# Optimization experiments

Hardware: AMD Instinct MI355X
Metric: run time of the kernel (lower is better)

## Reference

```python
import jax, jax.numpy as jnp
import numpy as np

B, L, C = 2, 2048, 2048
H, HKV, D = 16, 4, 128  # heads, kv heads, head_dim
G = H // HKV            # GQA group size
NEG = -1e9


def rms_norm(x, w, eps=1e-6):
    # FastRMSNorm: compute in fp32, scale by weight, cast back
    xf = x.astype(jnp.float32)
    y = xf * jax.lax.rsqrt(jnp.mean(xf * xf, axis=-1, keepdims=True) + eps) * w
    return y.astype(x.dtype)


def apply_rope(t, cos, sin):
    # t: (B, h, L, D); cos/sin: (L, D//2) broadcast to (1,1,L,D//2)
    t1, t2 = jnp.split(t, 2, axis=-1)
    c = cos[None, None]
    s = sin[None, None]
    return jnp.concatenate([t1 * c - t2 * s, t2 * c + t1 * s], axis=-1)


def setup_inputs() -> dict:
    key = jax.random.key(0)
    ks = jax.random.split(key, 8)
    x = jax.random.normal(ks[0], (B, L, C), jnp.float32)
    Wq = jax.random.normal(ks[1], (H * D, C), jnp.float32) * 0.02
    Wk = jax.random.normal(ks[2], (HKV * D, C), jnp.float32) * 0.02
    Wv = jax.random.normal(ks[3], (HKV * D, C), jnp.float32) * 0.02
    Wo = jax.random.normal(ks[4], (C, H * D), jnp.float32) * 0.02
    q_norm_w = jnp.ones((D,), jnp.float32)
    k_norm_w = jnp.ones((D,), jnp.float32)
    pos = jnp.arange(L, dtype=jnp.float32)[:, None]
    inv_freq = 1.0 / (10000.0 ** (jnp.arange(0, D, 2, dtype=jnp.float32) / D))
    ang = pos * inv_freq[None, :]            # (L, D//2)
    rope_cos = jnp.cos(ang)
    rope_sin = jnp.sin(ang)
    # VAR-style block-causal visibility: 8 blocks of 256, query block i sees key blocks <= i
    blk = jnp.arange(L) // 256
    vis = blk[None, :] <= blk[:, None]       # (L, L) bool
    attn_bias = jnp.where(vis, 0.0, NEG).astype(jnp.float32)[None, None]  # (1,1,L,L)
    return dict(x=x, Wq=Wq, Wk=Wk, Wv=Wv, Wo=Wo, q_norm_w=q_norm_w,
                k_norm_w=k_norm_w, rope_cos=rope_cos, rope_sin=rope_sin,
                attn_bias=attn_bias)


def reference(x, Wq, Wk, Wv, Wo, q_norm_w, k_norm_w, rope_cos, rope_sin, attn_bias):
    b, l, c = x.shape
    # fused projections -> (B, h, L, D)
    q = rms_norm((x @ Wq.T).reshape(b, l, H, D), q_norm_w).transpose(0, 2, 1, 3)
    k = rms_norm((x @ Wk.T).reshape(b, l, HKV, D), k_norm_w).transpose(0, 2, 1, 3)
    v = (x @ Wv.T).reshape(b, l, HKV, D).transpose(0, 2, 1, 3)
    q = apply_rope(q, rope_cos, rope_sin)
    k = apply_rope(k, rope_cos, rope_sin)
    scale = D ** -0.5
    # GQA: group query heads over kv heads
    qg = q.reshape(b, HKV, G, l, D)
    scores = jnp.einsum('bkgqd,bkKd->bkgqK', qg, k) * scale
    scores = scores + attn_bias[:, :, None]  # broadcast (1,1,1,L,L)
    probs = jax.nn.softmax(scores, axis=-1)
    out = jnp.einsum('bkgqK,bkKd->bkgqd', probs, v)
    out = out.reshape(b, H, l, D).transpose(0, 2, 1, 3).reshape(b, l, H * D)
    return out @ Wo.T
```

## Files before the change

### kernel.cpp

```cpp
#include <hip/hip_runtime.h>

#define B_ 2
#define L_ 2048
#define C_ 2048
#define H_ 16
#define HKV_ 4
#define D_ 128
#define G_ (H_ / HKV_)
#define TOK_ (B_ * L_)
#define NQKV_ 3072

typedef __bf16 bf16;
typedef __bf16 bf16x4 __attribute__((ext_vector_type(4)));
typedef __bf16 bf16x8 __attribute__((ext_vector_type(8)));
typedef float f32x4 __attribute__((ext_vector_type(4)));

__device__ inline void gload16(const void* g, void* l) {
  __builtin_amdgcn_global_load_lds(
      (const __attribute__((address_space(1))) void*)g,
      (__attribute__((address_space(3))) void*)l, 16, 0, 0);
}

__global__ void cvt_bf16(const float* __restrict__ in, bf16* __restrict__ out, int n4) {
  int stride = gridDim.x * blockDim.x;
  for (int j = blockIdx.x * blockDim.x + threadIdx.x; j < n4; j += stride) {
    float4 v = reinterpret_cast<const float4*>(in)[j];
    bf16x4 o = {(bf16)v.x, (bf16)v.y, (bf16)v.z, (bf16)v.w};
    reinterpret_cast<bf16x4*>(out)[j] = o;
  }
}

template <bool OUT_F32>
__global__ __launch_bounds__(256) void gemm_bt(
    const bf16* __restrict__ A, const bf16* __restrict__ Bm,
    void* __restrict__ Cm, int M, int N, int K) {
  __shared__ __align__(16) bf16 sA[128 * 32];
  __shared__ __align__(16) bf16 sB[128 * 32];
  const int tid = threadIdx.x;
  const int row0 = blockIdx.x * 128, col0 = blockIdx.y * 128;
  const int wid = tid >> 6, lane = tid & 63;
  const int wr = wid >> 1, wc = wid & 1;
  const int l15 = lane & 15, kk = (lane >> 4) * 8;
  f32x4 acc[4][4] = {};
  const int nk = K / 32;
  const int f0 = tid;
  const int r0 = f0 >> 2, c0 = f0 & 3;
  const int f1 = 256 + tid;
  const int r1 = f1 >> 2, c1 = f1 & 3;
  const int ldsA0 = (wid * 64) * 8, ldsA1 = (256 + wid * 64) * 8;
  for (int kt = 0; kt < nk; ++kt) {
    __syncthreads();
    gload16(A + (size_t)(row0 + r0) * K + kt * 32 + c0 * 8, sA + ldsA0);
    gload16(A + (size_t)(row0 + r1) * K + kt * 32 + c1 * 8, sA + ldsA1);
    gload16(Bm + (size_t)(col0 + r0) * K + kt * 32 + c0 * 8, sB + ldsA0);
    gload16(Bm + (size_t)(col0 + r1) * K + kt * 32 + c1 * 8, sB + ldsA1);
    __syncthreads();
    bf16x8 af[4], bfr[4];
#pragma unroll
    for (int m = 0; m < 4; ++m)
      af[m] = *reinterpret_cast<const bf16x8*>(sA + (wr * 64 + m * 16 + l15) * 32 + kk);
#pragma unroll
    for (int n = 0; n < 4; ++n)
      bfr[n] = *reinterpret_cast<const bf16x8*>(sB + (wc * 64 + n * 16 + l15) * 32 + kk);
#pragma unroll
    for (int m = 0; m < 4; ++m)
#pragma unroll
      for (int n = 0; n < 4; ++n)
        acc[m][n] = __builtin_amdgcn_mfma_f32_16x16x32_bf16(af[m], bfr[n], acc[m][n], 0, 0, 0);
  }
#pragma unroll
  for (int m = 0; m < 4; ++m)
#pragma unroll
    for (int n = 0; n < 4; ++n)
#pragma unroll
      for (int r = 0; r < 4; ++r) {
        int row = row0 + wr * 64 + m * 16 + (lane >> 4) * 4 + r;
        int col = col0 + wc * 64 + n * 16 + l15;
        if constexpr (OUT_F32)
          reinterpret_cast<float*>(Cm)[(size_t)row * N + col] = acc[m][n][r];
        else
          reinterpret_cast<bf16*>(Cm)[(size_t)row * N + col] = (bf16)acc[m][n][r];
      }
}

__global__ void k_norm_rope(const bf16* __restrict__ proj,
                            const float* __restrict__ normw,
                            const float* __restrict__ cosb,
                            const float* __restrict__ sinb,
                            bf16* __restrict__ out) {
  int wid = (blockIdx.x * blockDim.x + threadIdx.x) >> 6;
  int lane = threadIdx.x & 63;
  int head = wid & 3, tok = wid >> 2;
  int b = tok / L_, l = tok % L_;
  const bf16* p = proj + (size_t)tok * NQKV_ + H_ * D_ + head * D_;
  float t1 = (float)p[lane];
  float t2 = (float)p[lane + 64];
  float ss = t1 * t1 + t2 * t2;
#pragma unroll
  for (int off = 32; off; off >>= 1) ss += __shfl_xor(ss, off);
  float r = rsqrtf(ss * (1.0f / 128.0f) + 1e-6f);
  float n1 = t1 * r * normw[lane];
  float n2 = t2 * r * normw[lane + 64];
  float c = cosb[l * 64 + lane], s = sinb[l * 64 + lane];
  bf16* q = out + (((size_t)b * HKV_ + head) * L_ + l) * D_;
  q[lane] = (bf16)(n1 * c - n2 * s);
  q[lane + 64] = (bf16)(n2 * c + n1 * s);
}

__global__ __launch_bounds__(256) void v_transpose(const bf16* __restrict__ proj,
                                                   bf16* __restrict__ vt) {
  __shared__ __align__(16) bf16 sT[64 * 136];
  const int t = threadIdx.x;
  const int l0 = blockIdx.x * 64;
  const int bk = blockIdx.y;
  const bf16* src = proj + (size_t)((bk >> 2) * L_ + l0) * NQKV_ + (H_ + HKV_) * D_ + (bk & 3) * D_;
#pragma unroll
  for (int c = 0; c < 4; ++c) {
    int idx = c * 256 + t;
    int l = idx >> 4, dc = idx & 15;
    bf16x8 v = *reinterpret_cast<const bf16x8*>(src + (size_t)l * NQKV_ + dc * 8);
    *reinterpret_cast<bf16x8*>((char*)sT + l * 272 + ((dc ^ (l >> 3)) << 4)) = v;
  }
  __syncthreads();
  bf16* dst = vt + (size_t)bk * D_ * L_ + l0;
#pragma unroll
  for (int c = 0; c < 4; ++c) {
    int idx = c * 256 + t;
    int d = idx >> 3, lg = idx & 7;
    bf16x8 o;
#pragma unroll
    for (int j = 0; j < 8; ++j) {
      int l = lg * 8 + j;
      o[j] = *reinterpret_cast<const bf16*>((char*)sT + l * 272 + (((d >> 3) ^ lg) << 4) + (d & 7) * 2);
    }
    *reinterpret_cast<bf16x8*>(dst + (size_t)d * L_ + lg * 8) = o;
  }
}

__global__ __launch_bounds__(512, 4) void attn_fused(
    const bf16* __restrict__ QKV,
    const bf16* __restrict__ Kn,
    const bf16* __restrict__ Vt,
    const float* __restrict__ qnw,
    const float* __restrict__ cosb, const float* __restrict__ sinb,
    bf16* __restrict__ AO) {
  __shared__ __align__(16) bf16 sK[2][64 * 128];
  __shared__ __align__(16) bf16 sV[2][64 * 128];
  __shared__ __align__(16) bf16 sP[8 * 16 * 64];
  const int tid = threadIdx.x;
  const int wid = tid >> 6, lane = tid & 63;
  const int bid = blockIdx.x;
  const int bk = bid & 7;
  const int qt = (bid < 256) ? (bid >> 3) : 63 - ((bid - 256) >> 3);
  const int b = bk >> 2;
  const int hl = wid & 3, qs = wid >> 2;
  const int h = (bk & 3) * G_ + hl;
  const int qrow0 = qt * 32 + qs * 16;
  const int l15 = lane & 15, g4 = lane >> 4, kk = g4 * 8;
  const int swz = (l15 & 7) << 4;

  const int qrow = qrow0 + l15;
  const bf16* qsrc = QKV + (size_t)(b * L_ + qrow) * NQKV_ + h * D_;
  float t[4][8];
  float ss = 0.f;
#pragma unroll
  for (int c = 0; c < 4; ++c) {
    bf16x8 v = *reinterpret_cast<const bf16x8*>(qsrc + c * 32 + kk);
#pragma unroll
    for (int j = 0; j < 8; ++j) { t[c][j] = (float)v[j]; ss += t[c][j] * t[c][j]; }
  }

  const int kr0 = tid >> 4, kc0 = tid & 15;
  const int kr1 = 32 + kr0;
  const int vr0 = tid >> 3, vc0 = tid & 7;
  const int vr1 = 64 + vr0;
  const bf16* kb = Kn + (size_t)bk * L_ * D_;
  const bf16* vb = Vt + (size_t)bk * D_ * (size_t)L_;
  const bf16* kp0 = kb + (size_t)kr0 * D_ + ((kc0 ^ (kr0 & 7)) * 8);
  const bf16* kp1 = kb + (size_t)kr1 * D_ + ((kc0 ^ (kr1 & 7)) * 8);
  const bf16* vp0 = vb + (size_t)vr0 * L_ + ((vc0 ^ (vr0 & 7)) * 8);
  const bf16* vp1 = vb + (size_t)vr1 * L_ + ((vc0 ^ (vr1 & 7)) * 8);

  const int ntiles = ((qt >> 3) + 1) * 4;
  gload16(kp0, &sK[0][tid * 8]);
  gload16(kp1, &sK[0][(512 + tid) * 8]);
  gload16(vp0, &sV[0][tid * 8]);
  gload16(vp1, &sV[0][(512 + tid) * 8]);

  constexpr float SCL = 0.12752650038632816f;
  ss += __shfl_xor(ss, 16);
  ss += __shfl_xor(ss, 32);
  const float rr = rsqrtf(ss * (1.0f / 128.0f) + 1e-6f);
  bf16x8 qf[4];
#pragma unroll
  for (int c = 0; c < 2; ++c)
#pragma unroll
    for (int j = 0; j < 8; ++j) {
      int i = c * 32 + kk + j;
      float n1 = t[c][j] * rr * qnw[i];
      float n2 = t[c + 2][j] * rr * qnw[i + 64];
      float cs = cosb[qrow * 64 + i], sn = sinb[qrow * 64 + i];
      qf[c][j] = (bf16)((n1 * cs - n2 * sn) * SCL);
      qf[c + 2][j] = (bf16)((n2 * cs + n1 * sn) * SCL);
    }

  char* myP = (char*)(sP + wid * 16 * 64);
  f32x4 acc[8] = {};
  float mref = -1e30f, lpart = 0.f;

  __syncthreads();

  auto tile_step = [&](const bf16* sKc, const bf16* sVc, bf16* sKn_, bf16* sVn_,
                       int ktNext, bool doPref) {
    if (doPref) {
      gload16(kp0 + (size_t)ktNext * 64 * D_, &sKn_[tid * 8]);
      gload16(kp1 + (size_t)ktNext * 64 * D_, &sKn_[(512 + tid) * 8]);
      gload16(vp0 + ktNext * 64, &sVn_[tid * 8]);
      gload16(vp1 + ktNext * 64, &sVn_[(512 + tid) * 8]);
    }
    const char* cK = (const char*)sKc;
    const char* cV = (const char*)sVc;
    f32x4 s[4];
    __builtin_amdgcn_s_setprio(1);
#pragma unroll
    for (int n = 0; n < 4; ++n) {
      f32x4 st = {};
#pragma unroll
      for (int c = 0; c < 4; ++c) {
        int byte = (n * 16 + l15) * 256 + ((((c << 2) + g4) ^ (l15 & 7)) << 4);
        bf16x8 kf = *reinterpret_cast<const bf16x8*>(cK + byte);
        st = __builtin_amdgcn_mfma_f32_16x16x32_bf16(kf, qf[c], st, 0, 0, 0);
      }
      s[n] = st;
    }
    __builtin_amdgcn_s_setprio(0);
    float pm = fmaxf(fmaxf(s[0][0], s[0][1]), fmaxf(s[0][2], s[0][3]));
#pragma unroll
    for (int n = 1; n < 4; ++n)
      pm = fmaxf(pm, fmaxf(fmaxf(s[n][0], s[n][1]), fmaxf(s[n][2], s[n][3])));
    if (!__all(pm <= mref + 8.f)) {
      pm = fmaxf(pm, __shfl_xor(pm, 16));
      pm = fmaxf(pm, __shfl_xor(pm, 32));
      float mnew = fmaxf(mref, pm);
      float resc = exp2f(mref - mnew);
      mref = mnew;
      lpart *= resc;
#pragma unroll
      for (int f = 0; f < 8; ++f) acc[f] *= resc;
    }
#pragma unroll
    for (int n = 0; n < 4; ++n)
#pragma unroll
      for (int r = 0; r < 4; ++r) {
        float p = exp2f(s[n][r] - mref);
        s[n][r] = p;
        lpart += p;
      }
#pragma unroll
    for (int n = 0; n < 4; ++n) {
      bf16x4 pw = {(bf16)s[n][0], (bf16)s[n][1], (bf16)s[n][2], (bf16)s[n][3]};
      *reinterpret_cast<bf16x4*>(myP + l15 * 128 + (((n << 5) + (g4 << 3)) ^ swz)) = pw;
    }
    bf16x8 pf0 = *reinterpret_cast<const bf16x8*>(myP + l15 * 128 + ((g4 << 4) ^ swz));
    bf16x8 pf1 = *reinterpret_cast<const bf16x8*>(myP + l15 * 128 + ((64 + (g4 << 4)) ^ swz));
    __builtin_amdgcn_s_setprio(1);
#pragma unroll
    for (int f = 0; f < 8; ++f) {
      int d = f * 16 + l15;
      bf16x8 vf0 = *reinterpret_cast<const bf16x8*>(cV + d * 128 + ((g4 ^ (l15 & 7)) << 4));
      acc[f] = __builtin_amdgcn_mfma_f32_16x16x32_bf16(vf0, pf0, acc[f], 0, 0, 0);
      bf16x8 vf1 = *reinterpret_cast<const bf16x8*>(cV + d * 128 + (((4 + g4) ^ (l15 & 7)) << 4));
      acc[f] = __builtin_amdgcn_mfma_f32_16x16x32_bf16(vf1, pf1, acc[f], 0, 0, 0);
    }
    __builtin_amdgcn_s_setprio(0);
    __syncthreads();
  };

  for (int kt = 0; kt < ntiles; kt += 2) {
    tile_step(sK[0], sV[0], sK[1], sV[1], kt + 1, true);
    tile_step(sK[1], sV[1], sK[0], sV[0], kt + 2, kt + 2 < ntiles);
  }

  lpart += __shfl_xor(lpart, 16);
  lpart += __shfl_xor(lpart, 32);
  const float rinv = 1.f / lpart;
  bf16* aop = AO + ((size_t)(b * L_ + qrow0 + l15) * H_ + h) * D_ + (g4 << 2);
#pragma unroll
  for (int f = 0; f < 8; ++f) {
    bf16x4 o = {(bf16)(acc[f][0] * rinv), (bf16)(acc[f][1] * rinv),
                (bf16)(acc[f][2] * rinv), (bf16)(acc[f][3] * rinv)};
    *reinterpret_cast<bf16x4*>(aop + f * 16) = o;
  }
}

extern "C" void kernel_launch(void* const* d_in, const int* in_sizes, int n_in,
                              void* d_out, int out_size, void* d_ws, size_t ws_size,
                              hipStream_t stream) {
  const float* x = (const float*)d_in[0];
  const float* Wq = (const float*)d_in[1];
  const float* Wk = (const float*)d_in[2];
  const float* Wv = (const float*)d_in[3];
  const float* Wo = (const float*)d_in[4];
  const float* qnw = (const float*)d_in[5];
  const float* knw = (const float*)d_in[6];
  const float* rc = (const float*)d_in[7];
  const float* rs = (const float*)d_in[8];
  float* out = (float*)d_out;

  char* ws = (char*)d_ws;
  bf16* xb = (bf16*)ws;    ws += (size_t)TOK_ * C_ * 2;
  bf16* wqb = (bf16*)ws;   ws += (size_t)(H_ * D_) * C_ * 2;
  bf16* wkb = (bf16*)ws;   ws += (size_t)(HKV_ * D_) * C_ * 2;
  bf16* wvb = (bf16*)ws;   ws += (size_t)(HKV_ * D_) * C_ * 2;
  bf16* wob = (bf16*)ws;   ws += (size_t)C_ * (H_ * D_) * 2;
  bf16* qkv = (bf16*)ws;   ws += (size_t)TOK_ * NQKV_ * 2;
  bf16* Kb = (bf16*)ws;    ws += (size_t)TOK_ * HKV_ * D_ * 2;
  bf16* Vtb = (bf16*)ws;   ws += (size_t)TOK_ * HKV_ * D_ * 2;
  bf16* AOb = xb;

  auto cvt = [&](const float* src, bf16* dst, size_t n) {
    int n4 = (int)(n / 4);
    int grid = (n4 + 255) / 256;
    if (grid > 4096) grid = 4096;
    cvt_bf16<<<grid, 256, 0, stream>>>(src, dst, n4);
  };
  cvt(x, xb, (size_t)TOK_ * C_);
  cvt(Wq, wqb, (size_t)H_ * D_ * C_);
  cvt(Wk, wkb, (size_t)HKV_ * D_ * C_);
  cvt(Wv, wvb, (size_t)HKV_ * D_ * C_);
  cvt(Wo, wob, (size_t)C_ * H_ * D_);

  gemm_bt<false><<<dim3(TOK_ / 128, NQKV_ / 128), 256, 0, stream>>>(
      xb, wqb, qkv, TOK_, NQKV_, C_);

  k_norm_rope<<<(TOK_ * HKV_) / 4, 256, 0, stream>>>(qkv, knw, rc, rs, Kb);
  v_transpose<<<dim3(L_ / 64, B_ * HKV_), 256, 0, stream>>>(qkv, Vtb);

  attn_fused<<<512, 512, 0, stream>>>(qkv, Kb, Vtb, qnw, rc, rs, AOb);

  gemm_bt<true><<<dim3(TOK_ / 128, C_ / 128), 256, 0, stream>>>(
      AOb, wob, out, TOK_, C_, H_ * D_);
}
```

Before: 218.5 us.

## Rewrite GEMM with 256x128 tiles, triple-buffered async LDS loads, swizzled layout

The bf16 GEMM used for the QKV and output projections now uses 512-thread blocks with 256x128 tiles and a K step of 64. Global-to-LDS loads are triple-buffered and prefetched two steps ahead, with vmcnt waits replacing the two full syncthreads per iteration. The LDS layout uses an XOR swizzle to avoid bank conflicts, and MFMA sections get raised wave priority. This aims to hide memory latency and cut barrier overhead, at the cost of much more LDS (about 144KB) and fewer blocks in the grid.

Measured after the change: 232.9 us. 6.6% more time.

```diff
diff --git a/kernel.cpp b/kernel.cpp
--- a/kernel.cpp
+++ b/kernel.cpp
@@ -31,51 +31,80 @@
 }
 
 template <bool OUT_F32>
-__global__ __launch_bounds__(256) void gemm_bt(
+__global__ __launch_bounds__(512) void gemm_bt(
     const bf16* __restrict__ A, const bf16* __restrict__ Bm,
     void* __restrict__ Cm, int M, int N, int K) {
-  __shared__ __align__(16) bf16 sA[128 * 32];
-  __shared__ __align__(16) bf16 sB[128 * 32];
+  __shared__ __align__(16) bf16 sA[3][256 * 64];
+  __shared__ __align__(16) bf16 sB[3][128 * 64];
   const int tid = threadIdx.x;
-  const int row0 = blockIdx.x * 128, col0 = blockIdx.y * 128;
   const int wid = tid >> 6, lane = tid & 63;
-  const int wr = wid >> 1, wc = wid & 1;
-  const int l15 = lane & 15, kk = (lane >> 4) * 8;
+  const int row0 = blockIdx.x * 256, col0 = blockIdx.y * 128;
+  const int wwr = wid & 3, wwc = wid >> 2;
+  const int l15 = lane & 15, g4 = lane >> 4;
+  const int ra = tid >> 3, ca = tid & 7;
+  const bf16* gA = A + (size_t)(row0 + ra) * K + ((ca ^ (ra & 7)) << 3);
+  const bf16* gB = Bm + (size_t)(col0 + ra) * K + ((ca ^ (ra & 7)) << 3);
+  const int ldsOff = tid * 8;
+  const int nk = K >> 6;
+
+  auto stage = [&](int kt, int slot) {
+    const bf16* a = gA + kt * 64;
+    const bf16* b = gB + kt * 64;
+#pragma unroll
+    for (int j = 0; j < 4; ++j)
+      gload16(a + (size_t)(64 * j) * K, &sA[slot][ldsOff + j * 64 * 64]);
+#pragma unroll
+    for (int j = 0; j < 2; ++j)
+      gload16(b + (size_t)(64 * j) * K, &sB[slot][ldsOff + j * 64 * 64]);
+  };
+
   f32x4 acc[4][4] = {};
-  const int nk = K / 32;
-  const int f0 = tid;
-  const int r0 = f0 >> 2, c0 = f0 & 3;
-  const int f1 = 256 + tid;
-  const int r1 = f1 >> 2, c1 = f1 & 3;
-  const int ldsA0 = (wid * 64) * 8, ldsA1 = (256 + wid * 64) * 8;
+  stage(0, 0);
+  stage(1, 1);
+  asm volatile("s_waitcnt vmcnt(6)" ::: "memory");
+  __builtin_amdgcn_s_barrier();
+  __builtin_amdgcn_sched_barrier(0);
+
+  int slot = 0;
   for (int kt = 0; kt < nk; ++kt) {
-    __syncthreads();
-    gload16(A + (size_t)(row0 + r0) * K + kt * 32 + c0 * 8, sA + ldsA0);
-    gload16(A + (size_t)(row0 + r1) * K + kt * 32 + c1 * 8, sA + ldsA1);
-    gload16(Bm + (size_t)(col0 + r0) * K + kt * 32 + c0 * 8, sB + ldsA0);
-    gload16(Bm + (size_t)(col0 + r1) * K + kt * 32 + c1 * 8, sB + ldsA1);
-    __syncthreads();
-    bf16x8 af[4], bfr[4];
-#pragma unroll
-    for (int m = 0; m < 4; ++m)
-      af[m] = *reinterpret_cast<const bf16x8*>(sA + (wr * 64 + m * 16 + l15) * 32 + kk);
+    int s2 = slot + 2; if (s2 >= 3) s2 -= 3;
+    if (kt + 2 < nk) stage(kt + 2, s2);
+    const bf16* cA = sA[slot];
+    const bf16* cB = sB[slot];
+#pragma unroll
+    for (int kh = 0; kh < 2; ++kh) {
+      bf16x8 af[4], bfr[4];
+      const int ch = (((kh << 2) + g4) ^ (l15 & 7)) << 3;
+#pragma unroll
+      for (int m = 0; m < 4; ++m)
+        af[m] = *reinterpret_cast<const bf16x8*>(cA + (wwr * 64 + m * 16 + l15) * 64 + ch);
+#pragma unroll
+      for (int n = 0; n < 4; ++n)
+        bfr[n] = *reinterpret_cast<const bf16x8*>(cB + (wwc * 64 + n * 16 + l15) * 64 + ch);
+      __builtin_amdgcn_s_setprio(1);
+#pragma unroll
+      for (int m = 0; m < 4; ++m)
+#pragma unroll
+        for (int n = 0; n < 4; ++n)
+          acc[m][n] = __builtin_amdgcn_mfma_f32_16x16x32_bf16(af[m], bfr[n], acc[m][n], 0, 0, 0);
+      __builtin_amdgcn_s_setprio(0);
+    }
+    if (kt + 2 < nk)
+      asm volatile("s_waitcnt vmcnt(6)" ::: "memory");
+    else
+      asm volatile("s_waitcnt vmcnt(0)" ::: "memory");
+    __builtin_amdgcn_s_barrier();
+    __builtin_amdgcn_sched_barrier(0);
+    slot = (slot + 1 == 3) ? 0 : slot + 1;
+  }
+#pragma unroll
+  for (int m = 0; m < 4; ++m)
 #pragma unroll
     for (int n = 0; n < 4; ++n)
-      bfr[n] = *reinterpret_cast<const bf16x8*>(sB + (wc * 64 + n * 16 + l15) * 32 + kk);
-#pragma unroll
-    for (int m = 0; m < 4; ++m)
-#pragma unroll
-      for (int n = 0; n < 4; ++n)
-        acc[m][n] = __builtin_amdgcn_mfma_f32_16x16x32_bf16(af[m], bfr[n], acc[m][n], 0, 0, 0);
-  }
-#pragma unroll
-  for (int m = 0; m < 4; ++m)
-#pragma unroll
-    for (int n = 0; n < 4; ++n)
 #pragma unroll
       for (int r = 0; r < 4; ++r) {
-        int row = row0 + wr * 64 + m * 16 + (lane >> 4) * 4 + r;
-        int col = col0 + wc * 64 + n * 16 + l15;
+        int row = row0 + wwr * 64 + m * 16 + g4 * 4 + r;
+        int col = col0 + wwc * 64 + n * 16 + l15;
         if constexpr (OUT_F32)
           reinterpret_cast<float*>(Cm)[(size_t)row * N + col] = acc[m][n][r];
         else
@@ -330,7 +359,7 @@
   cvt(Wv, wvb, (size_t)HKV_ * D_ * C_);
   cvt(Wo, wob, (size_t)C_ * H_ * D_);
 
-  gemm_bt<false><<<dim3(TOK_ / 128, NQKV_ / 128), 256, 0, stream>>>(
+  gemm_bt<false><<<dim3(TOK_ / 256, NQKV_ / 128), 512, 0, stream>>>(
       xb, wqb, qkv, TOK_, NQKV_, C_);
 
   k_norm_rope<<<(TOK_ * HKV_) / 4, 256, 0, stream>>>(qkv, knw, rc, rs, Kb);
@@ -338,6 +367,6 @@
 
   attn_fused<<<512, 512, 0, stream>>>(qkv, Kb, Vtb, qnw, rc, rs, AOb);
 
-  gemm_bt<true><<<dim3(TOK_ / 128, C_ / 128), 256, 0, stream>>>(
+  gemm_bt<true><<<dim3(TOK_ / 256, C_ / 128), 512, 0, stream>>>(
       AOb, wob, out, TOK_, C_, H_ * D_);
 }
```

## Triple-buffer GEMM LDS tiles with async prefetch two stages ahead

Applied to the files above, without the earlier changes.

The bf16 GEMM used for the QKV and output projections now keeps three LDS slots and issues global-to-LDS loads two K-steps ahead. Each step waits on its own stage with a counted vmcnt and a single barrier, so load latency can overlap the MFMA work instead of being serialized between two barriers. It also raises wave priority around the MFMA block and asks for three blocks per CU in the launch bounds. The cost is triple the LDS footprint per block and fragile hand-written waitcnt and barrier ordering.

After: 207.5 us. -5.0%, faster.

```diff
diff --git a/kernel.cpp b/kernel.cpp
--- a/kernel.cpp
+++ b/kernel.cpp
@@ -31,11 +31,11 @@
 }
 
 template <bool OUT_F32>
-__global__ __launch_bounds__(256) void gemm_bt(
+__global__ __launch_bounds__(256, 3) void gemm_bt(
     const bf16* __restrict__ A, const bf16* __restrict__ Bm,
     void* __restrict__ Cm, int M, int N, int K) {
-  __shared__ __align__(16) bf16 sA[128 * 32];
-  __shared__ __align__(16) bf16 sB[128 * 32];
+  __shared__ __align__(16) bf16 sA[3][128 * 32];
+  __shared__ __align__(16) bf16 sB[3][128 * 32];
   const int tid = threadIdx.x;
   const int row0 = blockIdx.x * 128, col0 = blockIdx.y * 128;
   const int wid = tid >> 6, lane = tid & 63;
@@ -43,30 +43,50 @@
   const int l15 = lane & 15, kk = (lane >> 4) * 8;
   f32x4 acc[4][4] = {};
   const int nk = K / 32;
-  const int f0 = tid;
-  const int r0 = f0 >> 2, c0 = f0 & 3;
-  const int f1 = 256 + tid;
-  const int r1 = f1 >> 2, c1 = f1 & 3;
+  const int r0 = tid >> 2, c0 = tid & 3;
+  const int r1 = 64 + r0, c1 = c0;
   const int ldsA0 = (wid * 64) * 8, ldsA1 = (256 + wid * 64) * 8;
+
+  auto stage = [&](int kt, int slot) {
+    gload16(A + (size_t)(row0 + r0) * K + kt * 32 + c0 * 8, &sA[slot][ldsA0]);
+    gload16(A + (size_t)(row0 + r1) * K + kt * 32 + c1 * 8, &sA[slot][ldsA1]);
+    gload16(Bm + (size_t)(col0 + r0) * K + kt * 32 + c0 * 8, &sB[slot][ldsA0]);
+    gload16(Bm + (size_t)(col0 + r1) * K + kt * 32 + c1 * 8, &sB[slot][ldsA1]);
+  };
+
+  stage(0, 0);
+  stage(1, 1);
+  asm volatile("s_waitcnt vmcnt(4)" ::: "memory");
+  __builtin_amdgcn_s_barrier();
+  __builtin_amdgcn_sched_barrier(0);
+
+  int slot = 0;
   for (int kt = 0; kt < nk; ++kt) {
-    __syncthreads();
-    gload16(A + (size_t)(row0 + r0) * K + kt * 32 + c0 * 8, sA + ldsA0);
-    gload16(A + (size_t)(row0 + r1) * K + kt * 32 + c1 * 8, sA + ldsA1);
-    gload16(Bm + (size_t)(col0 + r0) * K + kt * 32 + c0 * 8, sB + ldsA0);
-    gload16(Bm + (size_t)(col0 + r1) * K + kt * 32 + c1 * 8, sB + ldsA1);
-    __syncthreads();
+    int s2 = slot + 2; if (s2 >= 3) s2 -= 3;
+    if (kt + 2 < nk) stage(kt + 2, s2);
+    const bf16* cA = sA[slot];
+    const bf16* cB = sB[slot];
     bf16x8 af[4], bfr[4];
 #pragma unroll
     for (int m = 0; m < 4; ++m)
-      af[m] = *reinterpret_cast<const bf16x8*>(sA + (wr * 64 + m * 16 + l15) * 32 + kk);
+      af[m] = *reinterpret_cast<const bf16x8*>(cA + (wr * 64 + m * 16 + l15) * 32 + kk);
 #pragma unroll
     for (int n = 0; n < 4; ++n)
-      bfr[n] = *reinterpret_cast<const bf16x8*>(sB + (wc * 64 + n * 16 + l15) * 32 + kk);
+      bfr[n] = *reinterpret_cast<const bf16x8*>(cB + (wc * 64 + n * 16 + l15) * 32 + kk);
+    __builtin_amdgcn_s_setprio(1);
 #pragma unroll
     for (int m = 0; m < 4; ++m)
 #pragma unroll
       for (int n = 0; n < 4; ++n)
         acc[m][n] = __builtin_amdgcn_mfma_f32_16x16x32_bf16(af[m], bfr[n], acc[m][n], 0, 0, 0);
+    __builtin_amdgcn_s_setprio(0);
+    if (kt + 2 < nk)
+      asm volatile("s_waitcnt vmcnt(4)" ::: "memory");
+    else
+      asm volatile("s_waitcnt vmcnt(0)" ::: "memory");
+    __builtin_amdgcn_s_barrier();
+    __builtin_amdgcn_sched_barrier(0);
+    slot = (slot + 1 == 3) ? 0 : slot + 1;
   }
 #pragma unroll
   for (int m = 0; m < 4; ++m)
```
